# Kernel tuning notes

Measured on AMD Instinct MI355X. Metric: run time of the kernel, lower is better.

The kernel has to match this reference:

```python
import jax, jax.numpy as jnp
import numpy as np

B, N, K = 512, 256, 20  # graphs, nodes per graph, kNN neighbors


def _knn_idx(xg, k):
    # xg: [B, N, d] -> indices of k nearest neighbors (excluding self): [B, N, k]
    sq = jnp.sum(xg * xg, axis=-1)                       # [B, N]
    d2 = sq[:, :, None] + sq[:, None, :] - 2.0 * jnp.einsum('bnd,bmd->bnm', xg, xg)
    d2 = d2 + jnp.eye(xg.shape[1], dtype=xg.dtype)[None] * 1e9  # no self-loops
    _, idx = jax.lax.top_k(-d2, k)
    return idx


def _edge_conv(xg, idx, mlp):
    # gather neighbor features x_j: [B, N, K, d]
    x_j = jax.vmap(lambda xb, ib: xb[ib])(xg, idx)
    x_i = jnp.broadcast_to(xg[:, :, None, :], x_j.shape)
    t = jnp.concatenate([x_i, x_j - x_i], axis=-1)       # [B, N, K, 2d]
    msg = mlp(t)
    return jnp.max(msg, axis=2)                           # max aggregation over neighbors


def setup_inputs() -> dict:
    key = jax.random.key(0)
    ks = jax.random.split(key, 16)
    s = 0.1
    inp = {
        'x': jax.random.normal(ks[0], (B * N, 2), jnp.float32),
        'batch': jnp.repeat(jnp.arange(B, dtype=jnp.int64), N),
        'c1_w0': jax.random.normal(ks[1], (4, 16), jnp.float32) * s,
        'c1_b0': jnp.zeros((16,), jnp.float32),
        'c1_w1': jax.random.normal(ks[2], (16, 16), jnp.float32) * s,
        'c1_b1': jnp.zeros((16,), jnp.float32),
        'c1_w2': jax.random.normal(ks[3], (16, 16), jnp.float32) * s,
        'c1_b2': jnp.zeros((16,), jnp.float32),
        'c2_w0': jax.random.normal(ks[4], (32, 32), jnp.float32) * s,
        'c2_b0': jnp.zeros((32,), jnp.float32),
        'lin1_w': jax.random.normal(ks[5], (48, 128), jnp.float32) * s,
        'lin1_b': jnp.zeros((128,), jnp.float32),
        'm_w0': jax.random.normal(ks[6], (128, 64), jnp.float32) * s,
        'm_b0': jnp.zeros((64,), jnp.float32),
        'm_w1': jax.random.normal(ks[7], (64, 64), jnp.float32) * s,
        'm_b1': jnp.zeros((64,), jnp.float32),
        'm_w2': jax.random.normal(ks[8], (64, 1), jnp.float32) * s,
        'm_b2': jnp.zeros((1,), jnp.float32),
    }
    return inp


def reference(x, batch, c1_w0, c1_b0, c1_w1, c1_b1, c1_w2, c1_b2,
              c2_w0, c2_b0, lin1_w, lin1_b,
              m_w0, m_b0, m_w1, m_b1, m_w2, m_b2):
    xg = x.reshape(B, N, -1)  # batch ids are sorted, N nodes per graph

    # conv1: dynamic kNN on raw features, edge MLP [4,16,16,16] (plain last layer)
    def mlp1(t):
        h = jax.nn.relu(t @ c1_w0 + c1_b0)
        h = jax.nn.relu(h @ c1_w1 + c1_b1)
        return h @ c1_w2 + c1_b2
    x1 = _edge_conv(xg, _knn_idx(xg, K), mlp1)            # [B, N, 16]

    # conv2: dynamic kNN recomputed on x1, edge MLP [32,32]
    def mlp2(t):
        return t @ c2_w0 + c2_b0
    x2 = _edge_conv(x1, _knn_idx(x1, K), mlp2)            # [B, N, 32]

    out = jnp.concatenate([x1, x2], axis=-1) @ lin1_w + lin1_b  # [B, N, 128]
    pooled = jnp.max(out, axis=1)                          # global max pool -> [B, 128]

    h = jax.nn.relu(pooled @ m_w0 + m_b0)                  # dropout inactive at eval
    h = jax.nn.relu(h @ m_w1 + m_b1)
    return h @ m_w2 + m_b2                                 # [B, 1]
```

## Files before the change

### kernel.cpp

```cpp
#include <hip/hip_runtime.h>
#include <float.h>

#define NN 256
#define KK 20

__device__ __forceinline__ float med3f(float a, float b, float c) {
    return __builtin_amdgcn_fmed3f(a, b, c);
}

__device__ __forceinline__ float dist2d(const float* __restrict__ s_xyq,
                                        float xi0, float xi1, float sqi,
                                        int j, int t) {
    float4 q = ((const float4*)s_xyq)[j];
    float dot = xi0*q.x + xi1*q.y;
    float d = (sqi + q.z) - 2.0f*dot;
    return (j == t) ? __builtin_inff() : d;
}

__device__ __forceinline__ float dist16f(const float* __restrict__ s_x1,
                                         const float* __restrict__ s_sq,
                                         const float* __restrict__ x1f,
                                         float sq2, int j, int t) {
    const float4* xp = (const float4*)(s_x1 + (j << 4));
    float4 q0 = xp[0], q1 = xp[1], q2 = xp[2], q3 = xp[3];
    float dot;
    dot  = x1f[0]*q0.x;  dot += x1f[1]*q0.y;  dot += x1f[2]*q0.z;  dot += x1f[3]*q0.w;
    dot += x1f[4]*q1.x;  dot += x1f[5]*q1.y;  dot += x1f[6]*q1.z;  dot += x1f[7]*q1.w;
    dot += x1f[8]*q2.x;  dot += x1f[9]*q2.y;  dot += x1f[10]*q2.z; dot += x1f[11]*q2.w;
    dot += x1f[12]*q3.x; dot += x1f[13]*q3.y; dot += x1f[14]*q3.z; dot += x1f[15]*q3.w;
    float d = (sq2 + s_sq[j]) - 2.0f*dot;
    return (j == t) ? __builtin_inff() : d;
}

__global__ __launch_bounds__(256, 1)
void Net_35055523070563_kernel(
    const float* __restrict__ x,
    const float* __restrict__ c1_w0, const float* __restrict__ c1_b0,
    const float* __restrict__ c1_w1, const float* __restrict__ c1_b1,
    const float* __restrict__ c1_w2, const float* __restrict__ c1_b2,
    const float* __restrict__ c2_w0, const float* __restrict__ c2_b0,
    const float* __restrict__ lin1_w, const float* __restrict__ lin1_b,
    const float* __restrict__ m_w0, const float* __restrict__ m_b0,
    const float* __restrict__ m_w1, const float* __restrict__ m_b1,
    const float* __restrict__ m_w2, const float* __restrict__ m_b2,
    float* __restrict__ out)
{
    __shared__ __align__(16) float R[9216];
    __shared__ unsigned char s_ki[(KK + 1) * NN];
    __shared__ float s_w0d[32], s_w0b[32], s_b0[16], s_b1[16], s_b2[16];
    __shared__ __align__(16) float s_W1[256], s_W2[256];
    __shared__ __align__(16) float s_wtd[512], s_wb[512], s_bc[32];
    __shared__ float s_part[128], s_pooled[128], s_head[64];

    float* s_xyq = R;
    float* s_v   = R;
    float* s_sq  = R;
    float* s_x1  = R + 5120;
    float* c2t   = R;
    float* shW   = R;
    unsigned char* LeqB = (unsigned char*)(R + 1024);

    const int t = threadIdx.x;
    const int b = blockIdx.x;

    float2 xv = ((const float2*)x)[b*NN + t];
    float sq0 = xv.x*xv.x + xv.y*xv.y;
    s_xyq[t*4+0] = xv.x; s_xyq[t*4+1] = xv.y; s_xyq[t*4+2] = sq0; s_xyq[t*4+3] = 0.f;
    if (t < 16) { s_b0[t] = c1_b0[t]; s_b1[t] = c1_b1[t]; s_b2[t] = c1_b2[t]; }
    if (t < 32) {
        int r = t >> 4, c = t & 15;
        float wt = c1_w0[r*16+c], wb = c1_w0[(2+r)*16+c];
        s_w0d[t] = wt - wb; s_w0b[t] = wb;
    }
    s_W1[t] = c1_w1[t]; s_W2[t] = c1_w2[t];
    if (t < 32) s_bc[t] = c2_b0[t];
    #pragma unroll
    for (int it = 0; it < 2; ++it) {
        int e = t + it*NN; int k = e >> 5, c = e & 31;
        float wt = c2_w0[k*32+c], wb = c2_w0[(16+k)*32+c];
        s_wtd[e] = wt - wb; s_wb[e] = wb;
    }
    __syncthreads();

    {
        float r[KK];
        #pragma unroll
        for (int k = 0; k < KK; ++k) r[k] = __builtin_inff();
        #pragma unroll 4
        for (int j = 0; j < NN; ++j) {
            float d = dist2d(s_xyq, xv.x, xv.y, sq0, j, t);
            #pragma unroll
            for (int k = KK-1; k >= 1; --k) r[k] = med3f(d, r[k-1], r[k]);
            r[0] = fminf(r[0], d);
        }
        float V = r[KK-1];
        int cntL = 0, cntE = 0;
        #pragma unroll 4
        for (int j = 0; j < NN; ++j) {
            float d = dist2d(s_xyq, xv.x, xv.y, sq0, j, t);
            s_ki[min(cntL, KK)*NN + t] = (unsigned char)j;
            cntL += (d < V) ? 1 : 0;
            if (d == V) { LeqB[min(cntE, 8)*NN + t] = (unsigned char)j; ++cntE; }
        }
        int need = KK - cntL;
        for (int e = 0; e < need; ++e)
            s_ki[(cntL + e)*NN + t] = LeqB[e*NN + t];
    }
    __syncthreads();

    float u[16];
    {
        #pragma unroll
        for (int c = 0; c < 16; ++c) {
            u[c] = s_b0[c] + xv.x*s_w0d[c] + xv.y*s_w0d[16+c];
            s_v[t*20 + c] = xv.x*s_w0b[c] + xv.y*s_w0b[16+c];
        }
    }
    __syncthreads();

    float x1f[16];
    {
        float acc[16];
        #pragma unroll
        for (int c = 0; c < 16; ++c) acc[c] = -FLT_MAX;
        #pragma unroll 1
        for (int p = 0; p < KK; p += 2) {
            int j0 = s_ki[p*NN + t], j1 = s_ki[(p+1)*NN + t];
            const float* va = s_v + j0*20;
            const float* vb = s_v + j1*20;
            float h1a[16], h1b[16];
            #pragma unroll
            for (int c = 0; c < 16; ++c) {
                h1a[c] = fmaxf(u[c] + va[c], 0.f);
                h1b[c] = fmaxf(u[c] + vb[c], 0.f);
            }
            float h2a[16], h2b[16];
            #pragma unroll
            for (int c = 0; c < 16; ++c) { h2a[c] = s_b1[c]; h2b[c] = s_b1[c]; }
            #pragma unroll
            for (int k = 0; k < 16; ++k) {
                float fa = h1a[k], fb = h1b[k];
                #pragma unroll
                for (int c = 0; c < 16; ++c) {
                    float w = s_W1[k*16+c];
                    h2a[c] = fmaf(fa, w, h2a[c]);
                    h2b[c] = fmaf(fb, w, h2b[c]);
                }
            }
            #pragma unroll
            for (int c = 0; c < 16; ++c) {
                h2a[c] = fmaxf(h2a[c], 0.f); h2b[c] = fmaxf(h2b[c], 0.f);
                h1a[c] = s_b2[c];            h1b[c] = s_b2[c];
            }
            #pragma unroll
            for (int k = 0; k < 16; ++k) {
                float fa = h2a[k], fb = h2b[k];
                #pragma unroll
                for (int c = 0; c < 16; ++c) {
                    float w = s_W2[k*16+c];
                    h1a[c] = fmaf(fa, w, h1a[c]);
                    h1b[c] = fmaf(fb, w, h1b[c]);
                }
            }
            #pragma unroll
            for (int c = 0; c < 16; ++c)
                acc[c] = fmaxf(acc[c], fmaxf(h1a[c], h1b[c]));
        }
        #pragma unroll
        for (int c = 0; c < 16; ++c) { s_x1[t*16 + c] = acc[c]; x1f[c] = acc[c]; }
    }
    float sq2 = 0.f;
    #pragma unroll
    for (int c = 0; c < 16; ++c) sq2 += x1f[c]*x1f[c];
    __syncthreads();
    s_sq[t] = sq2;
    __syncthreads();

    {
        float r[KK];
        #pragma unroll
        for (int k = 0; k < KK; ++k) r[k] = __builtin_inff();
        #pragma unroll 2
        for (int j = 0; j < NN; ++j) {
            float d = dist16f(s_x1, s_sq, x1f, sq2, j, t);
            #pragma unroll
            for (int k = KK-1; k >= 1; --k) r[k] = med3f(d, r[k-1], r[k]);
            r[0] = fminf(r[0], d);
        }
        float V = r[KK-1];
        int cntL = 0, cntE = 0;
        #pragma unroll 2
        for (int j = 0; j < NN; ++j) {
            float d = dist16f(s_x1, s_sq, x1f, sq2, j, t);
            s_ki[min(cntL, KK)*NN + t] = (unsigned char)j;
            cntL += (d < V) ? 1 : 0;
            if (d == V) { LeqB[min(cntE, 8)*NN + t] = (unsigned char)j; ++cntE; }
        }
        int need = KK - cntL;
        for (int e = 0; e < need; ++e)
            s_ki[(cntL + e)*NN + t] = LeqB[e*NN + t];
    }
    __syncthreads();

    float x2f[32];
    {
        float cj[32];
        #pragma unroll
        for (int c = 0; c < 32; ++c) cj[c] = 0.f;
        #pragma unroll
        for (int k = 0; k < 16; ++k) {
            float fk = x1f[k];
            #pragma unroll
            for (int c = 0; c < 32; ++c) cj[c] = fmaf(fk, s_wb[k*32+c], cj[c]);
        }
        #pragma unroll
        for (int c = 0; c < 32; ++c) c2t[c*NN + t] = cj[c];
        float ar[32];
        #pragma unroll
        for (int c = 0; c < 32; ++c) ar[c] = s_bc[c];
        #pragma unroll
        for (int k = 0; k < 16; ++k) {
            float fk = x1f[k];
            #pragma unroll
            for (int c = 0; c < 32; ++c) ar[c] = fmaf(fk, s_wtd[k*32+c], ar[c]);
        }
        __syncthreads();
        float mx[32];
        #pragma unroll
        for (int c = 0; c < 32; ++c) mx[c] = -FLT_MAX;
        #pragma unroll 1
        for (int p = 0; p < KK; ++p) {
            int j = s_ki[p*NN + t];
            #pragma unroll
            for (int c = 0; c < 32; ++c) mx[c] = fmaxf(mx[c], c2t[c*NN + j]);
        }
        #pragma unroll
        for (int c = 0; c < 32; ++c) x2f[c] = ar[c] + mx[c];
    }
    __syncthreads();

    for (int cc = 0; cc < 4; ++cc) {
        #pragma unroll
        for (int it = 0; it < 6; ++it) {
            int e = t + it*NN; int r = e >> 5, c = e & 31;
            shW[e] = lin1_w[r*128 + cc*32 + c];
        }
        __syncthreads();
        float accL[32];
        #pragma unroll
        for (int c = 0; c < 32; ++c) accL[c] = lin1_b[cc*32 + c];
        #pragma unroll
        for (int k = 0; k < 48; ++k) {
            float fk = (k < 16) ? x1f[k] : x2f[k-16];
            #pragma unroll
            for (int c = 0; c < 32; ++c) accL[c] = fmaf(fk, shW[k*32+c], accL[c]);
        }
        #pragma unroll
        for (int m = 1; m < 64; m <<= 1) {
            #pragma unroll
            for (int c = 0; c < 32; ++c)
                accL[c] = fmaxf(accL[c], __shfl_xor(accL[c], m, 64));
        }
        int w = t >> 6, lane = t & 63;
        if (lane == 0) {
            #pragma unroll
            for (int c = 0; c < 32; ++c) s_part[w*32 + c] = accL[c];
        }
        __syncthreads();
        if (t < 32) {
            float m0 = fmaxf(fmaxf(s_part[t], s_part[32+t]),
                             fmaxf(s_part[64+t], s_part[96+t]));
            s_pooled[cc*32 + t] = m0;
        }
        __syncthreads();
    }

    if (t < 64) {
        float s = m_b0[t];
        #pragma unroll 8
        for (int k = 0; k < 128; ++k) s = fmaf(s_pooled[k], m_w0[k*64 + t], s);
        s_head[t] = fmaxf(s, 0.f);
    }
    __syncthreads();
    if (t < 64) {
        float s = m_b1[t];
        #pragma unroll 8
        for (int k = 0; k < 64; ++k) s = fmaf(s_head[k], m_w1[k*64 + t], s);
        s = fmaxf(s, 0.f);
        float v = s * m_w2[t];
        #pragma unroll
        for (int m = 1; m < 64; m <<= 1) v += __shfl_xor(v, m, 64);
        if (t == 0) out[b] = v + m_b2[0];
    }
}

extern "C" void kernel_launch(void* const* d_in, const int* in_sizes, int n_in,
                              void* d_out, int out_size, void* d_ws, size_t ws_size,
                              hipStream_t stream) {
    const float* x    = (const float*)d_in[0];
    const float* c1w0 = (const float*)d_in[2];
    const float* c1b0 = (const float*)d_in[3];
    const float* c1w1 = (const float*)d_in[4];
    const float* c1b1 = (const float*)d_in[5];
    const float* c1w2 = (const float*)d_in[6];
    const float* c1b2 = (const float*)d_in[7];
    const float* c2w0 = (const float*)d_in[8];
    const float* c2b0 = (const float*)d_in[9];
    const float* l1w  = (const float*)d_in[10];
    const float* l1b  = (const float*)d_in[11];
    const float* mw0  = (const float*)d_in[12];
    const float* mb0  = (const float*)d_in[13];
    const float* mw1  = (const float*)d_in[14];
    const float* mb1  = (const float*)d_in[15];
    const float* mw2  = (const float*)d_in[16];
    const float* mb2  = (const float*)d_in[17];
    float* out = (float*)d_out;
    hipLaunchKernelGGL(Net_35055523070563_kernel, dim3(512), dim3(256), 0, stream,
                       x, c1w0, c1b0, c1w1, c1b1, c1w2, c1b2, c2w0, c2b0,
                       l1w, l1b, mw0, mb0, mw1, mb1, mw2, mb2, out);
}
```

Baseline: 636.7 us.

## Split fused kernel into three kernels for kNN1/conv1, kNN2/conv2/lin1, and head

Splits the single monolithic per-graph kernel into three launches: conv1 with its kNN writing x1 to workspace, conv2 with its kNN plus lin1 and pooling writing pooled features to workspace, and a small MLP head kernel. Each kernel needs fewer registers and less shared memory, which may let the compiler schedule better or allow more resident blocks. In exchange it adds global round-trips for x1 (8 MB) and the pooled features, plus two extra launch overheads.

After: 520.0 us. 1.22x faster.

```diff
diff --git a/kernel.cpp b/kernel.cpp
--- a/kernel.cpp
+++ b/kernel.cpp
@@ -33,31 +33,19 @@
 }
 
 __global__ __launch_bounds__(256, 1)
-void Net_35055523070563_kernel(
-    const float* __restrict__ x,
-    const float* __restrict__ c1_w0, const float* __restrict__ c1_b0,
-    const float* __restrict__ c1_w1, const float* __restrict__ c1_b1,
-    const float* __restrict__ c1_w2, const float* __restrict__ c1_b2,
-    const float* __restrict__ c2_w0, const float* __restrict__ c2_b0,
-    const float* __restrict__ lin1_w, const float* __restrict__ lin1_b,
-    const float* __restrict__ m_w0, const float* __restrict__ m_b0,
-    const float* __restrict__ m_w1, const float* __restrict__ m_b1,
-    const float* __restrict__ m_w2, const float* __restrict__ m_b2,
-    float* __restrict__ out)
+void k1_knn1_conv1(const float* __restrict__ x,
+                   const float* __restrict__ c1_w0, const float* __restrict__ c1_b0,
+                   const float* __restrict__ c1_w1, const float* __restrict__ c1_b1,
+                   const float* __restrict__ c1_w2, const float* __restrict__ c1_b2,
+                   float* __restrict__ x1out)
 {
-    __shared__ __align__(16) float R[9216];
+    __shared__ __align__(16) float R[5120];
     __shared__ unsigned char s_ki[(KK + 1) * NN];
     __shared__ float s_w0d[32], s_w0b[32], s_b0[16], s_b1[16], s_b2[16];
     __shared__ __align__(16) float s_W1[256], s_W2[256];
-    __shared__ __align__(16) float s_wtd[512], s_wb[512], s_bc[32];
-    __shared__ float s_part[128], s_pooled[128], s_head[64];
 
     float* s_xyq = R;
     float* s_v   = R;
-    float* s_sq  = R;
-    float* s_x1  = R + 5120;
-    float* c2t   = R;
-    float* shW   = R;
     unsigned char* LeqB = (unsigned char*)(R + 1024);
 
     const int t = threadIdx.x;
@@ -73,13 +61,6 @@
         s_w0d[t] = wt - wb; s_w0b[t] = wb;
     }
     s_W1[t] = c1_w1[t]; s_W2[t] = c1_w2[t];
-    if (t < 32) s_bc[t] = c2_b0[t];
-    #pragma unroll
-    for (int it = 0; it < 2; ++it) {
-        int e = t + it*NN; int k = e >> 5, c = e & 31;
-        float wt = c2_w0[k*32+c], wb = c2_w0[(16+k)*32+c];
-        s_wtd[e] = wt - wb; s_wb[e] = wb;
-    }
     __syncthreads();
 
     {
@@ -109,71 +90,108 @@
     __syncthreads();
 
     float u[16];
-    {
+    #pragma unroll
+    for (int c = 0; c < 16; ++c) {
+        u[c] = s_b0[c] + xv.x*s_w0d[c] + xv.y*s_w0d[16+c];
+        s_v[t*20 + c] = xv.x*s_w0b[c] + xv.y*s_w0b[16+c];
+    }
+    __syncthreads();
+
+    float acc[16];
+    #pragma unroll
+    for (int c = 0; c < 16; ++c) acc[c] = -FLT_MAX;
+    #pragma unroll 1
+    for (int p = 0; p < KK; p += 2) {
+        int j0 = s_ki[p*NN + t], j1 = s_ki[(p+1)*NN + t];
+        const float* va = s_v + j0*20;
+        const float* vb = s_v + j1*20;
+        float h1a[16], h1b[16];
         #pragma unroll
         for (int c = 0; c < 16; ++c) {
-            u[c] = s_b0[c] + xv.x*s_w0d[c] + xv.y*s_w0d[16+c];
-            s_v[t*20 + c] = xv.x*s_w0b[c] + xv.y*s_w0b[16+c];
-        }
-    }
-    __syncthreads();
+            h1a[c] = fmaxf(u[c] + va[c], 0.f);
+            h1b[c] = fmaxf(u[c] + vb[c], 0.f);
+        }
+        float h2a[16], h2b[16];
+        #pragma unroll
+        for (int c = 0; c < 16; ++c) { h2a[c] = s_b1[c]; h2b[c] = s_b1[c]; }
+        #pragma unroll
+        for (int k = 0; k < 16; ++k) {
+            float fa = h1a[k], fb = h1b[k];
+            #pragma unroll
+            for (int c = 0; c < 16; ++c) {
+                float w = s_W1[k*16+c];
+                h2a[c] = fmaf(fa, w, h2a[c]);
+                h2b[c] = fmaf(fb, w, h2b[c]);
+            }
+        }
+        #pragma unroll
+        for (int c = 0; c < 16; ++c) {
+            h2a[c] = fmaxf(h2a[c], 0.f); h2b[c] = fmaxf(h2b[c], 0.f);
+            h1a[c] = s_b2[c];            h1b[c] = s_b2[c];
+        }
+        #pragma unroll
+        for (int k = 0; k < 16; ++k) {
+            float fa = h2a[k], fb = h2b[k];
+            #pragma unroll
+            for (int c = 0; c < 16; ++c) {
+                float w = s_W2[k*16+c];
+                h1a[c] = fmaf(fa, w, h1a[c]);
+                h1b[c] = fmaf(fb, w, h1b[c]);
+            }
+        }
+        #pragma unroll
+        for (int c = 0; c < 16; ++c)
+            acc[c] = fmaxf(acc[c], fmaxf(h1a[c], h1b[c]));
+    }
+    float4* o = (float4*)(x1out + (b*NN + t)*16);
+    o[0] = make_float4(acc[0],  acc[1],  acc[2],  acc[3]);
+    o[1] = make_float4(acc[4],  acc[5],  acc[6],  acc[7]);
+    o[2] = make_float4(acc[8],  acc[9],  acc[10], acc[11]);
+    o[3] = make_float4(acc[12], acc[13], acc[14], acc[15]);
+}
+
+__global__ __launch_bounds__(256, 1)
+void k2_knn2_conv2_lin1(const float* __restrict__ x1in,
+                        const float* __restrict__ c2_w0, const float* __restrict__ c2_b0,
+                        const float* __restrict__ lin1_w, const float* __restrict__ lin1_b,
+                        float* __restrict__ pooled)
+{
+    __shared__ __align__(16) float R[8192];
+    __shared__ unsigned char s_ki[(KK + 1) * NN];
+    __shared__ float s_sq[NN];
+    __shared__ __align__(16) float s_wtd[512], s_wb[512], s_bc[32];
+    __shared__ float s_part[128];
+
+    float* s_x1 = R;
+    float* c2t  = R;
+    float* shW  = R;
+    unsigned char* LeqB = (unsigned char*)(R + 4096);
+
+    const int t = threadIdx.x;
+    const int b = blockIdx.x;
 
     float x1f[16];
     {
-        float acc[16];
-        #pragma unroll
-        for (int c = 0; c < 16; ++c) acc[c] = -FLT_MAX;
-        #pragma unroll 1
-        for (int p = 0; p < KK; p += 2) {
-            int j0 = s_ki[p*NN + t], j1 = s_ki[(p+1)*NN + t];
-            const float* va = s_v + j0*20;
-            const float* vb = s_v + j1*20;
-            float h1a[16], h1b[16];
-            #pragma unroll
-            for (int c = 0; c < 16; ++c) {
-                h1a[c] = fmaxf(u[c] + va[c], 0.f);
-                h1b[c] = fmaxf(u[c] + vb[c], 0.f);
-            }
-            float h2a[16], h2b[16];
-            #pragma unroll
-            for (int c = 0; c < 16; ++c) { h2a[c] = s_b1[c]; h2b[c] = s_b1[c]; }
-            #pragma unroll
-            for (int k = 0; k < 16; ++k) {
-                float fa = h1a[k], fb = h1b[k];
-                #pragma unroll
-                for (int c = 0; c < 16; ++c) {
-                    float w = s_W1[k*16+c];
-                    h2a[c] = fmaf(fa, w, h2a[c]);
-                    h2b[c] = fmaf(fb, w, h2b[c]);
-                }
-            }
-            #pragma unroll
-            for (int c = 0; c < 16; ++c) {
-                h2a[c] = fmaxf(h2a[c], 0.f); h2b[c] = fmaxf(h2b[c], 0.f);
-                h1a[c] = s_b2[c];            h1b[c] = s_b2[c];
-            }
-            #pragma unroll
-            for (int k = 0; k < 16; ++k) {
-                float fa = h2a[k], fb = h2b[k];
-                #pragma unroll
-                for (int c = 0; c < 16; ++c) {
-                    float w = s_W2[k*16+c];
-                    h1a[c] = fmaf(fa, w, h1a[c]);
-                    h1b[c] = fmaf(fb, w, h1b[c]);
-                }
-            }
-            #pragma unroll
-            for (int c = 0; c < 16; ++c)
-                acc[c] = fmaxf(acc[c], fmaxf(h1a[c], h1b[c]));
-        }
-        #pragma unroll
-        for (int c = 0; c < 16; ++c) { s_x1[t*16 + c] = acc[c]; x1f[c] = acc[c]; }
+        const float4* ip = (const float4*)(x1in + (b*NN + t)*16);
+        float4 a0 = ip[0], a1 = ip[1], a2 = ip[2], a3 = ip[3];
+        x1f[0]=a0.x; x1f[1]=a0.y; x1f[2]=a0.z; x1f[3]=a0.w;
+        x1f[4]=a1.x; x1f[5]=a1.y; x1f[6]=a1.z; x1f[7]=a1.w;
+        x1f[8]=a2.x; x1f[9]=a2.y; x1f[10]=a2.z; x1f[11]=a2.w;
+        x1f[12]=a3.x; x1f[13]=a3.y; x1f[14]=a3.z; x1f[15]=a3.w;
+        float4* sp = (float4*)(s_x1 + t*16);
+        sp[0]=a0; sp[1]=a1; sp[2]=a2; sp[3]=a3;
     }
     float sq2 = 0.f;
     #pragma unroll
     for (int c = 0; c < 16; ++c) sq2 += x1f[c]*x1f[c];
-    __syncthreads();
     s_sq[t] = sq2;
+    if (t < 32) s_bc[t] = c2_b0[t];
+    #pragma unroll
+    for (int it = 0; it < 2; ++it) {
+        int e = t + it*NN; int k = e >> 5, c = e & 31;
+        float wt = c2_w0[k*32+c], wb = c2_w0[(16+k)*32+c];
+        s_wtd[e] = wt - wb; s_wb[e] = wb;
+    }
     __syncthreads();
 
     {
@@ -239,6 +257,7 @@
     }
     __syncthreads();
 
+    #pragma unroll 1
     for (int cc = 0; cc < 4; ++cc) {
         #pragma unroll
         for (int it = 0; it < 6; ++it) {
@@ -270,28 +289,38 @@
         if (t < 32) {
             float m0 = fmaxf(fmaxf(s_part[t], s_part[32+t]),
                              fmaxf(s_part[64+t], s_part[96+t]));
-            s_pooled[cc*32 + t] = m0;
+            pooled[b*128 + cc*32 + t] = m0;
         }
         __syncthreads();
     }
-
-    if (t < 64) {
-        float s = m_b0[t];
-        #pragma unroll 8
-        for (int k = 0; k < 128; ++k) s = fmaf(s_pooled[k], m_w0[k*64 + t], s);
-        s_head[t] = fmaxf(s, 0.f);
-    }
-    __syncthreads();
-    if (t < 64) {
-        float s = m_b1[t];
-        #pragma unroll 8
-        for (int k = 0; k < 64; ++k) s = fmaf(s_head[k], m_w1[k*64 + t], s);
-        s = fmaxf(s, 0.f);
-        float v = s * m_w2[t];
-        #pragma unroll
-        for (int m = 1; m < 64; m <<= 1) v += __shfl_xor(v, m, 64);
-        if (t == 0) out[b] = v + m_b2[0];
-    }
+}
+
+__global__ __launch_bounds__(64, 1)
+void k3_head(const float* __restrict__ pooled,
+             const float* __restrict__ m_w0, const float* __restrict__ m_b0,
+             const float* __restrict__ m_w1, const float* __restrict__ m_b1,
+             const float* __restrict__ m_w2, const float* __restrict__ m_b2,
+             float* __restrict__ out)
+{
+    __shared__ float s_p[128], s_head[64];
+    const int t = threadIdx.x;
+    const int b = blockIdx.x;
+    s_p[t]      = pooled[b*128 + t];
+    s_p[t + 64] = pooled[b*128 + 64 + t];
+    __syncthreads();
+    float s = m_b0[t];
+    #pragma unroll 8
+    for (int k = 0; k < 128; ++k) s = fmaf(s_p[k], m_w0[k*64 + t], s);
+    s_head[t] = fmaxf(s, 0.f);
+    __syncthreads();
+    s = m_b1[t];
+    #pragma unroll 8
+    for (int k = 0; k < 64; ++k) s = fmaf(s_head[k], m_w1[k*64 + t], s);
+    s = fmaxf(s, 0.f);
+    float v = s * m_w2[t];
+    #pragma unroll
+    for (int m = 1; m < 64; m <<= 1) v += __shfl_xor(v, m, 64);
+    if (t == 0) out[b] = v + m_b2[0];
 }
 
 extern "C" void kernel_launch(void* const* d_in, const int* in_sizes, int n_in,
@@ -315,7 +344,15 @@
     const float* mw2  = (const float*)d_in[16];
     const float* mb2  = (const float*)d_in[17];
     float* out = (float*)d_out;
-    hipLaunchKernelGGL(Net_35055523070563_kernel, dim3(512), dim3(256), 0, stream,
-                       x, c1w0, c1b0, c1w1, c1b1, c1w2, c1b2, c2w0, c2b0,
-                       l1w, l1b, mw0, mb0, mw1, mb1, mw2, mb2, out);
-}
+
+    float* ws     = (float*)d_ws;
+    float* x1buf  = ws;
+    float* plbuf  = ws + (size_t)512*256*16;
+
+    hipLaunchKernelGGL(k1_knn1_conv1, dim3(512), dim3(256), 0, stream,
+                       x, c1w0, c1b0, c1w1, c1b1, c1w2, c1b2, x1buf);
+    hipLaunchKernelGGL(k2_knn2_conv2_lin1, dim3(512), dim3(256), 0, stream,
+                       x1buf, c2w0, c2b0, l1w, l1b, plbuf);
+    hipLaunchKernelGGL(k3_head, dim3(512), dim3(64), 0, stream,
+                       plbuf, mw0, mb0, mw1, mb1, mw2, mb2, out);
+}
```
